# Kernel optimization log

Measured on AMD Instinct MI355X. Metric: run time of the kernel, lower is better.

Reference implementation:

```python
import jax, jax.numpy as jnp
import numpy as np

EPS_LN = 1e-6  # ieps_ln_default


def setup_inputs() -> dict:
    key = jax.random.key(0)
    ks = jax.random.split(key, 8)
    B, S, H, ID = 8, 2048, 8, 256  # batch, seq, heads, i_head_dim
    OD = 256                        # o_head_dim
    sc_hid = 1.0 / np.sqrt(2 * ID)
    sc_og = 1.0 / np.sqrt(ID + OD)
    return {
        "heads_input": jax.random.normal(ks[0], (B, S, H, ID), dtype=jnp.float32),
        "W_hid": jax.random.uniform(ks[1], (3 * OD, 2 * ID), jnp.float32, -sc_hid, sc_hid),
        "b_hid": jnp.zeros((3 * OD,), jnp.float32),
        "W_og": jax.random.uniform(ks[2], (OD, ID + OD), jnp.float32, -sc_og, sc_og),
        "b_og": jnp.zeros((OD,), jnp.float32),
        "ln_w": jnp.ones((H, ID), jnp.float32),
        "ln_b": jnp.zeros((H, ID), jnp.float32),
        "init_cx": jnp.zeros((H, OD), jnp.float32),
    }


def _forward(heads_input, W_hid, b_hid, W_og, b_og, ln_w, ln_b, init_cx):
    B, S, H, ID = heads_input.shape
    OD = init_cx.shape[-1]
    # RS1cumsumstatnorm: causal running sum, LayerNorm over (heads, dim) jointly
    csum = jnp.cumsum(heads_input, axis=1)
    mean = jnp.mean(csum, axis=(-2, -1), keepdims=True)
    var = jnp.var(csum, axis=(-2, -1), keepdims=True)
    csum = (csum - mean) * jax.lax.rsqrt(var + EPS_LN) * ln_w + ln_b
    # trans_hid on cat(input, csum): [B,S,H,2*ID] -> [B,S,H,3*OD]
    x2 = jnp.concatenate([heads_input, csum], axis=-1)
    g = jnp.einsum('bshd,od->bsho', x2, W_hid) + b_hid
    g = g.reshape(B, S, H, 3, OD)
    igate, fgate, hidden = g[..., 0, :], g[..., 1, :], g[..., 2, :]
    fgate = jax.nn.sigmoid(fgate)
    igh = jax.nn.sigmoid(igate) * jax.nn.relu(hidden)
    # LGateFunc: cell_t = f_t * cell_{t-1} + igh_t, starting from init_cx
    c0 = jnp.broadcast_to(init_cx, (B, H, OD))

    def step(c, fi):
        f, ig = fi
        c = f * c + ig
        return c, c

    _, cells = jax.lax.scan(step, c0, (jnp.moveaxis(fgate, 1, 0), jnp.moveaxis(igh, 1, 0)))
    cell = jnp.moveaxis(cells, 0, 1)  # [B,S,H,OD]
    # output gate on cat(input, cell)
    xo = jnp.concatenate([heads_input, cell], axis=-1)
    og = jax.nn.sigmoid(jnp.einsum('bshd,od->bsho', xo, W_og) + b_og)
    return og * cell


def reference(heads_input, W_hid, b_hid, W_og, b_og, ln_w, ln_b, init_cx):
    return _forward(heads_input, W_hid, b_hid, W_og, b_og, ln_w, ln_b, init_cx)
```

## Files before the change

kernel.cpp:

```cpp
#include <hip/hip_runtime.h>

typedef unsigned short u16;
typedef unsigned int u32;

typedef __attribute__((ext_vector_type(8))) short bf16x8;
typedef __attribute__((ext_vector_type(4))) float f32x4;

#define B_ 8
#define S_ 2048
#define H_ 8
#define ID_ 256
#define OD_ 256
#define K_ 512
#define M_ (B_*S_*H_)
#define N1_ 768
#define N2_ 256
#define G2_ 512

#define CSCH 64
#define CSST (S_/CSCH)

#define OFF_X2   (0ull)
#define SZ_X2    ((unsigned long long)M_*K_*2)
#define OFF_G    (OFF_X2 + SZ_X2)
#define SZ_G     ((unsigned long long)M_*G2_*2)
#define OFF_WH   (OFF_G + SZ_G)
#define SZ_WH    ((unsigned long long)N1_*K_*2)
#define OFF_WO   (OFF_WH + SZ_WH)
#define SZ_WO    ((unsigned long long)N2_*K_*2)
#define OFF_AUX  (OFF_WO + SZ_WO)
#define SZ_AUX   ((unsigned long long)B_*CSCH*2048*4)
#define OFF_CF   (OFF_AUX + SZ_AUX)
#define SZ_CARR  ((unsigned long long)B_*H_*32*256*4)
#define OFF_CC   (OFF_CF + SZ_CARR)
#define OFF_CIN  (OFF_CC + SZ_CARR)
#define OFF_BR   (OFF_CIN + SZ_CARR)
#define SZ_BR    ((unsigned long long)N1_*4)

__device__ __forceinline__ u16 f2bf(float f) {
    union { float f; u32 u; } v; v.f = f;
    u32 u = v.u;
    u += 0x7fffu + ((u >> 16) & 1u);
    return (u16)(u >> 16);
}
__device__ __forceinline__ float bf2f(u16 h) {
    union { u32 u; float f; } v; v.u = ((u32)h) << 16;
    return v.f;
}
__device__ __forceinline__ u32 pack2h(float a, float b) {
    union { _Float16 h; u16 u; } x, y;
    x.h = (_Float16)a; y.h = (_Float16)b;
    return (u32)x.u | ((u32)y.u << 16);
}
__device__ __forceinline__ float h2f(u16 u) {
    union { u16 u; _Float16 h; } v; v.u = u;
    return (float)v.h;
}
__device__ __forceinline__ float sigm(float x) {
    return 1.0f / (1.0f + __expf(-x));
}

__device__ __forceinline__ void gld16(const void* g, void* l) {
    __builtin_amdgcn_global_load_lds(
        (const __attribute__((address_space(1))) void*)g,
        (__attribute__((address_space(3))) void*)l, 16, 0, 0);
}

__device__ __forceinline__ int whid_src_row(int n) {
    if (n < 512) {
        int o = ((n >> 7) << 6) + ((n & 127) >> 1);
        return (n & 1) ? (512 + o) : o;
    }
    return 256 + (n - 512);
}

__global__ __launch_bounds__(256) void wconv_kernel(
    const float* __restrict__ Whid, const float* __restrict__ bhid,
    const float* __restrict__ Wog,
    u16* __restrict__ WhB, u16* __restrict__ WoB, float* __restrict__ br)
{
    int idx = blockIdx.x * 256 + threadIdx.x;
    if (idx < N1_*K_) {
        const int n = idx >> 9, k = idx & 511;
        WhB[idx] = f2bf(Whid[(size_t)whid_src_row(n) * K_ + k]);
    }
    if (idx < N2_*K_) WoB[idx] = f2bf(Wog[idx]);
    if (idx < N1_) br[idx] = bhid[whid_src_row(idx)];
}

__global__ __launch_bounds__(256) void csum_phase1(
    const float* __restrict__ X, float* __restrict__ aux)
{
    const int bch = blockIdx.x;
    const int b = bch / CSCH, ch = bch % CSCH;
    const int t = threadIdx.x;
    float acc[8];
#pragma unroll
    for (int h = 0; h < 8; ++h) acc[h] = 0.f;
    for (int i = 0; i < CSST; ++i) {
        const int s = ch * CSST + i;
        const float* xp = X + ((size_t)(b * S_ + s)) * 2048 + t;
#pragma unroll
        for (int h = 0; h < 8; ++h) acc[h] += xp[h * 256];
    }
    float* ap = aux + (size_t)bch * 2048 + t;
#pragma unroll
    for (int h = 0; h < 8; ++h) ap[h * 256] = acc[h];
}

__global__ __launch_bounds__(256) void csum_mid(float* __restrict__ aux)
{
    const int idx = blockIdx.x * 256 + threadIdx.x;
    const int b = idx >> 11, c = idx & 2047;
    float run = 0.f;
    for (int ch = 0; ch < CSCH; ++ch) {
        float* p = aux + ((size_t)(b * CSCH + ch)) * 2048 + c;
        float v = *p; *p = run; run += v;
    }
}

__global__ __launch_bounds__(256) void csum_phase2(
    const float* __restrict__ X, const float* __restrict__ aux,
    const float* __restrict__ lnw, const float* __restrict__ lnb,
    u16* __restrict__ x2)
{
    const int bch = blockIdx.x;
    const int b = bch / CSCH, ch = bch % CSCH;
    const int t = threadIdx.x;
    float c[8], wv[8], bv[8];
#pragma unroll
    for (int h = 0; h < 8; ++h) {
        c[h]  = aux[(size_t)bch * 2048 + h * 256 + t];
        wv[h] = lnw[h * 256 + t];
        bv[h] = lnb[h * 256 + t];
    }
    __shared__ float red[2][4];
    for (int i = 0; i < CSST; ++i) {
        const int s = ch * CSST + i;
        const float* xp = X + ((size_t)(b * S_ + s)) * 2048 + t;
        float xa[8];
#pragma unroll
        for (int h = 0; h < 8; ++h) { xa[h] = xp[h * 256]; c[h] += xa[h]; }
        float sx = 0.f, sq = 0.f;
#pragma unroll
        for (int h = 0; h < 8; ++h) { sx += c[h]; sq += c[h] * c[h]; }
#pragma unroll
        for (int off = 32; off >= 1; off >>= 1) {
            sx += __shfl_down(sx, (unsigned)off);
            sq += __shfl_down(sq, (unsigned)off);
        }
        const int wid = t >> 6;
        if ((t & 63) == 0) { red[0][wid] = sx; red[1][wid] = sq; }
        __syncthreads();
        const float tsx = red[0][0] + red[0][1] + red[0][2] + red[0][3];
        const float tsq = red[1][0] + red[1][1] + red[1][2] + red[1][3];
        __syncthreads();
        const float mean = tsx * (1.f / 2048.f);
        const float var  = tsq * (1.f / 2048.f) - mean * mean;
        const float rstd = rsqrtf(var + 1e-6f);
        const size_t mrow = ((size_t)(b * S_ + s)) * H_;
#pragma unroll
        for (int h = 0; h < 8; ++h) {
            u16* row = x2 + (mrow + h) * (size_t)K_;
            row[t]       = f2bf(xa[h]);
            row[256 + t] = f2bf((c[h] - mean) * rstd * wv[h] + bv[h]);
        }
    }
}

template<int N, int EPI>
__global__ __launch_bounds__(256) void gemm_kernel(
    const u16* __restrict__ A, const u16* __restrict__ Bw,
    u16* __restrict__ Gout, const float* __restrict__ bias,
    const u16* __restrict__ cellbuf, float* __restrict__ Out)
{
    constexpr int NT = N / 128;
    const int blk = blockIdx.x;
    const int xcd = blk & 7;
    const int j = blk >> 3;
    const int tileN = j % NT;
    const int tileM = (j / NT) * 8 + xcd;
    const int m0 = tileM * 128, n0 = tileN * 128;
    const int tid = threadIdx.x;
    const int lane = tid & 63;
    const int w = tid >> 6, wm = w & 1, wn = w >> 1;
    const int l15 = lane & 15, quad = lane >> 4;

    __shared__ __align__(16) u16 smem[2 * 128 * 64];
    u16* As = smem;
    u16* Bs = smem + 128 * 64;

    const int lane3 = lane >> 3;
    const int pc = lane & 7;
    const int ra7 = l15 & 7;

    f32x4 acc[4][4];
    const f32x4 zero4 = {0.f, 0.f, 0.f, 0.f};
#pragma unroll
    for (int i = 0; i < 4; ++i)
#pragma unroll
        for (int jj = 0; jj < 4; ++jj) acc[i][jj] = zero4;

    for (int kt = 0; kt < K_ / 64; ++kt) {
        const int k0 = kt * 64;
#pragma unroll
        for (int p = 0; p < 4; ++p) {
            const int R0 = w * 32 + p * 8;
            const int r = R0 + lane3;
            const int ca = (pc ^ (r & 7)) * 8;
            gld16(A  + (size_t)(m0 + r) * K_ + k0 + ca, As + R0 * 64);
            gld16(Bw + (size_t)(n0 + r) * K_ + k0 + ca, Bs + R0 * 64);
        }
        asm volatile("s_waitcnt vmcnt(0)" ::: "memory");
        __syncthreads();
#pragma unroll
        for (int kk = 0; kk < 2; ++kk) {
            bf16x8 af[4], bfr[4];
#pragma unroll
            for (int i = 0; i < 4; ++i) {
                const int rowa = wm * 64 + i * 16 + l15;
                const int rowb = wn * 64 + i * 16 + l15;
                const int ca = ((kk * 4 + quad) ^ ra7) * 8;
                af[i]  = *(const bf16x8*)(const void*)(&As[rowa * 64 + ca]);
                bfr[i] = *(const bf16x8*)(const void*)(&Bs[rowb * 64 + ca]);
            }
#pragma unroll
            for (int i = 0; i < 4; ++i)
#pragma unroll
                for (int jj = 0; jj < 4; ++jj)
                    acc[i][jj] = __builtin_amdgcn_mfma_f32_16x16x32_bf16(
                        af[i], bfr[jj], acc[i][jj], 0, 0, 0);
        }
        __syncthreads();
    }

    float* Cf = (float*)smem;
    const int col4 = (tid & 31) * 4;
    float4 b4;
    if (EPI == 0) b4 = *(const float4*)(const void*)(bias + n0 + col4);
    else          b4 = *(const float4*)(const void*)(bias + n0 + col4);
#pragma unroll
    for (int half = 0; half < 2; ++half) {
        if (wm == half) {
#pragma unroll
            for (int i = 0; i < 4; ++i) {
                const int lrow0 = i * 16 + quad * 4;
#pragma unroll
                for (int jj = 0; jj < 4; ++jj) {
                    const int col = wn * 64 + jj * 16 + l15;
#pragma unroll
                    for (int r = 0; r < 4; ++r)
                        Cf[(lrow0 + r) * 128 + col] = acc[i][jj][r];
                }
            }
        }
        __syncthreads();
#pragma unroll
        for (int q = 0; q < 8; ++q) {
            const int lrow = q * 8 + (tid >> 5);
            const int grow = m0 + half * 64 + lrow;
            float4 v = *(const float4*)(const void*)(&Cf[lrow * 128 + col4]);
            if (EPI == 0) {
                if (tileN < 4) {
                    const float ig0 = sigm(v.x + b4.x) * fmaxf(v.y + b4.y, 0.f);
                    const float ig1 = sigm(v.z + b4.z) * fmaxf(v.w + b4.w, 0.f);
                    *(u32*)(void*)(Gout + (size_t)grow * G2_ + tileN * 64 + (col4 >> 1))
                        = pack2h(ig0, ig1);
                } else {
                    uint2 pk;
                    pk.x = pack2h(sigm(v.x + b4.x), sigm(v.y + b4.y));
                    pk.y = pack2h(sigm(v.z + b4.z), sigm(v.w + b4.w));
                    *(uint2*)(void*)(Gout + (size_t)grow * G2_ + 256 + (tileN - 4) * 128 + col4)
                        = pk;
                }
            } else {
                const u16* cp = cellbuf + (size_t)grow * K_ + 256 + n0 + col4;
                float4 o;
                o.x = sigm(v.x + b4.x) * bf2f(cp[0]);
                o.y = sigm(v.y + b4.y) * bf2f(cp[1]);
                o.z = sigm(v.z + b4.z) * bf2f(cp[2]);
                o.w = sigm(v.w + b4.w) * bf2f(cp[3]);
                *(float4*)(void*)(Out + (size_t)grow * N2_ + n0 + col4) = o;
            }
        }
        __syncthreads();
    }
}

__global__ __launch_bounds__(256) void scan_phase1(
    const u16* __restrict__ g2, float* __restrict__ cF, float* __restrict__ cC)
{
    const int blk = blockIdx.x;
    const int chp = blk & 7, bh = blk >> 3;
    const int h = bh & 7, b = bh >> 3;
    const int t = threadIdx.x;
    const int ch = chp * 4 + (t >> 6);
    const int o = (t & 63) * 4;
    float F[4] = {1.f, 1.f, 1.f, 1.f};
    float c[4] = {0.f, 0.f, 0.f, 0.f};
    for (int i = 0; i < 64; ++i) {
        const int s = ch * 64 + i;
        const size_t m = ((size_t)(b * S_ + s)) * H_ + h;
        const u16* gp = g2 + m * G2_;
        const uint2 igp = *(const uint2*)(const void*)(gp + o);
        const uint2 fgp = *(const uint2*)(const void*)(gp + 256 + o);
        const float f0 = h2f((u16)fgp.x), f1 = h2f((u16)(fgp.x >> 16));
        const float f2 = h2f((u16)fgp.y), f3 = h2f((u16)(fgp.y >> 16));
        c[0] = f0 * c[0] + h2f((u16)igp.x);        F[0] *= f0;
        c[1] = f1 * c[1] + h2f((u16)(igp.x >> 16)); F[1] *= f1;
        c[2] = f2 * c[2] + h2f((u16)igp.y);        F[2] *= f2;
        c[3] = f3 * c[3] + h2f((u16)(igp.y >> 16)); F[3] *= f3;
    }
    const size_t idx = ((size_t)(bh * 32 + ch)) * 256 + o;
    *(float4*)(void*)(cF + idx) = make_float4(F[0], F[1], F[2], F[3]);
    *(float4*)(void*)(cC + idx) = make_float4(c[0], c[1], c[2], c[3]);
}

__global__ __launch_bounds__(256) void scan_mid(
    const float* __restrict__ cF, const float* __restrict__ cC,
    const float* __restrict__ initcx, float* __restrict__ cin)
{
    const int bh = blockIdx.x;
    const int h = bh & 7;
    const int o = threadIdx.x;
    float c = initcx[h * 256 + o];
    for (int ch = 0; ch < 32; ++ch) {
        const size_t idx = ((size_t)(bh * 32 + ch)) * 256 + o;
        cin[idx] = c;
        c = cF[idx] * c + cC[idx];
    }
}

__global__ __launch_bounds__(256) void scan_phase2(
    const u16* __restrict__ g2, const float* __restrict__ cin,
    u16* __restrict__ x2)
{
    const int blk = blockIdx.x;
    const int chp = blk & 7, bh = blk >> 3;
    const int h = bh & 7, b = bh >> 3;
    const int t = threadIdx.x;
    const int ch = chp * 4 + (t >> 6);
    const int o = (t & 63) * 4;
    const size_t idx = ((size_t)(bh * 32 + ch)) * 256 + o;
    float4 c4 = *(const float4*)(const void*)(cin + idx);
    float c[4] = {c4.x, c4.y, c4.z, c4.w};
    for (int i = 0; i < 64; ++i) {
        const int s = ch * 64 + i;
        const size_t m = ((size_t)(b * S_ + s)) * H_ + h;
        const u16* gp = g2 + m * G2_;
        const uint2 igp = *(const uint2*)(const void*)(gp + o);
        const uint2 fgp = *(const uint2*)(const void*)(gp + 256 + o);
        const float f0 = h2f((u16)fgp.x), f1 = h2f((u16)(fgp.x >> 16));
        const float f2 = h2f((u16)fgp.y), f3 = h2f((u16)(fgp.y >> 16));
        c[0] = f0 * c[0] + h2f((u16)igp.x);
        c[1] = f1 * c[1] + h2f((u16)(igp.x >> 16));
        c[2] = f2 * c[2] + h2f((u16)igp.y);
        c[3] = f3 * c[3] + h2f((u16)(igp.y >> 16));
        uint2 pk;
        pk.x = (u32)f2bf(c[0]) | ((u32)f2bf(c[1]) << 16);
        pk.y = (u32)f2bf(c[2]) | ((u32)f2bf(c[3]) << 16);
        *(uint2*)(void*)(x2 + m * K_ + 256 + o) = pk;
    }
}

extern "C" void kernel_launch(void* const* d_in, const int* in_sizes, int n_in,
                              void* d_out, int out_size, void* d_ws, size_t ws_size,
                              hipStream_t stream)
{
    const float* X      = (const float*)d_in[0];
    const float* Whid   = (const float*)d_in[1];
    const float* bhid   = (const float*)d_in[2];
    const float* Wog    = (const float*)d_in[3];
    const float* bog    = (const float*)d_in[4];
    const float* lnw    = (const float*)d_in[5];
    const float* lnb    = (const float*)d_in[6];
    const float* initcx = (const float*)d_in[7];
    float* out = (float*)d_out;

    char* ws = (char*)d_ws;
    u16* x2   = (u16*)(ws + OFF_X2);
    u16* g    = (u16*)(ws + OFF_G);
    u16* WhB  = (u16*)(ws + OFF_WH);
    u16* WoB  = (u16*)(ws + OFF_WO);
    float* aux = (float*)(ws + OFF_AUX);
    float* cF  = (float*)(ws + OFF_CF);
    float* cC  = (float*)(ws + OFF_CC);
    float* cin = (float*)(ws + OFF_CIN);
    float* br  = (float*)(ws + OFF_BR);

    wconv_kernel<<<(N1_*K_ + 255) / 256, 256, 0, stream>>>(Whid, bhid, Wog, WhB, WoB, br);
    csum_phase1<<<B_ * CSCH, 256, 0, stream>>>(X, aux);
    csum_mid<<<64, 256, 0, stream>>>(aux);
    csum_phase2<<<B_ * CSCH, 256, 0, stream>>>(X, aux, lnw, lnb, x2);
    gemm_kernel<N1_, 0><<<(M_ / 128) * (N1_ / 128), 256, 0, stream>>>(
        x2, WhB, g, br, nullptr, nullptr);
    scan_phase1<<<B_ * H_ * 8, 256, 0, stream>>>(g, cF, cC);
    scan_mid<<<B_ * H_, 256, 0, stream>>>(cF, cC, initcx, cin);
    scan_phase2<<<B_ * H_ * 8, 256, 0, stream>>>(g, cin, x2);
    gemm_kernel<N2_, 1><<<(M_ / 128) * (N2_ / 128), 256, 0, stream>>>(
        x2, WoB, nullptr, bog, x2, out);
}
```

Baseline: 640.0 us.

## Write first GEMM epilogue straight from registers using permuted gate layout

```diff
diff --git a/kernel.cpp b/kernel.cpp
--- a/kernel.cpp
+++ b/kernel.cpp
@@ -34,8 +34,6 @@
 #define SZ_CARR  ((unsigned long long)B_*H_*32*256*4)
 #define OFF_CC   (OFF_CF + SZ_CARR)
 #define OFF_CIN  (OFF_CC + SZ_CARR)
-#define OFF_BR   (OFF_CIN + SZ_CARR)
-#define SZ_BR    ((unsigned long long)N1_*4)
 
 __device__ __forceinline__ u16 f2bf(float f) {
     union { float f; u32 u; } v; v.f = f;
@@ -67,17 +65,18 @@
 }
 
 __device__ __forceinline__ int whid_src_row(int n) {
-    if (n < 512) {
-        int o = ((n >> 7) << 6) + ((n & 127) >> 1);
-        return (n & 1) ? (512 + o) : o;
-    }
-    return 256 + (n - 512);
+    const int t = n >> 7, c = n & 127;
+    if (t < 4) {
+        const int wn = (c >> 6) & 1, jj = (c & 63) >> 4, l = c & 15;
+        const int o = t * 64 + wn * 32 + (jj & 1) * 16 + l;
+        return (jj < 2) ? o : (512 + o);
+    }
+    return 256 + (t - 4) * 128 + c;
 }
 
 __global__ __launch_bounds__(256) void wconv_kernel(
-    const float* __restrict__ Whid, const float* __restrict__ bhid,
-    const float* __restrict__ Wog,
-    u16* __restrict__ WhB, u16* __restrict__ WoB, float* __restrict__ br)
+    const float* __restrict__ Whid, const float* __restrict__ Wog,
+    u16* __restrict__ WhB, u16* __restrict__ WoB)
 {
     int idx = blockIdx.x * 256 + threadIdx.x;
     if (idx < N1_*K_) {
@@ -85,7 +84,6 @@
         WhB[idx] = f2bf(Whid[(size_t)whid_src_row(n) * K_ + k]);
     }
     if (idx < N2_*K_) WoB[idx] = f2bf(Wog[idx]);
-    if (idx < N1_) br[idx] = bhid[whid_src_row(idx)];
 }
 
 __global__ __launch_bounds__(256) void csum_phase1(
@@ -234,46 +232,67 @@
         __syncthreads();
     }
 
-    float* Cf = (float*)smem;
-    const int col4 = (tid & 31) * 4;
-    float4 b4;
-    if (EPI == 0) b4 = *(const float4*)(const void*)(bias + n0 + col4);
-    else          b4 = *(const float4*)(const void*)(bias + n0 + col4);
-#pragma unroll
-    for (int half = 0; half < 2; ++half) {
-        if (wm == half) {
+    if (EPI == 0) {
+        const int m_base = m0 + wm * 64 + quad * 4;
+        if (tileN < 4) {
+            const int o0 = tileN * 64 + wn * 32 + l15;
+            const float bI0 = bias[o0],        bI1 = bias[o0 + 16];
+            const float bH0 = bias[512 + o0],  bH1 = bias[512 + o0 + 16];
+            const int q = (tileN * 2 + wn) * 16 + l15;
 #pragma unroll
             for (int i = 0; i < 4; ++i) {
-                const int lrow0 = i * 16 + quad * 4;
-#pragma unroll
-                for (int jj = 0; jj < 4; ++jj) {
-                    const int col = wn * 64 + jj * 16 + l15;
-#pragma unroll
-                    for (int r = 0; r < 4; ++r)
-                        Cf[(lrow0 + r) * 128 + col] = acc[i][jj][r];
+#pragma unroll
+                for (int r = 0; r < 4; ++r) {
+                    const int m = m_base + i * 16 + r;
+                    const float ig0 = sigm(acc[i][0][r] + bI0) * fmaxf(acc[i][2][r] + bH0, 0.f);
+                    const float ig1 = sigm(acc[i][1][r] + bI1) * fmaxf(acc[i][3][r] + bH1, 0.f);
+                    *(u32*)(void*)(Gout + (size_t)m * G2_ + 2 * q) = pack2h(ig0, ig1);
                 }
             }
-        }
-        __syncthreads();
-#pragma unroll
-        for (int q = 0; q < 8; ++q) {
-            const int lrow = q * 8 + (tid >> 5);
-            const int grow = m0 + half * 64 + lrow;
-            float4 v = *(const float4*)(const void*)(&Cf[lrow * 128 + col4]);
-            if (EPI == 0) {
-                if (tileN < 4) {
-                    const float ig0 = sigm(v.x + b4.x) * fmaxf(v.y + b4.y, 0.f);
-                    const float ig1 = sigm(v.z + b4.z) * fmaxf(v.w + b4.w, 0.f);
-                    *(u32*)(void*)(Gout + (size_t)grow * G2_ + tileN * 64 + (col4 >> 1))
-                        = pack2h(ig0, ig1);
-                } else {
-                    uint2 pk;
-                    pk.x = pack2h(sigm(v.x + b4.x), sigm(v.y + b4.y));
-                    pk.y = pack2h(sigm(v.z + b4.z), sigm(v.w + b4.w));
-                    *(uint2*)(void*)(Gout + (size_t)grow * G2_ + 256 + (tileN - 4) * 128 + col4)
-                        = pk;
+        } else {
+            const int o0 = (tileN - 4) * 128 + wn * 64 + l15;
+            const float bF0 = bias[256 + o0],      bF1 = bias[256 + o0 + 16];
+            const float bF2 = bias[256 + o0 + 32], bF3 = bias[256 + o0 + 48];
+            const int qA = ((tileN - 4) * 4 + wn * 2) * 16 + l15;
+            const int qB = qA + 16;
+#pragma unroll
+            for (int i = 0; i < 4; ++i) {
+#pragma unroll
+                for (int r = 0; r < 4; ++r) {
+                    const int m = m_base + i * 16 + r;
+                    u16* row = Gout + (size_t)m * G2_ + 256;
+                    *(u32*)(void*)(row + 2 * qA) =
+                        pack2h(sigm(acc[i][0][r] + bF0), sigm(acc[i][1][r] + bF1));
+                    *(u32*)(void*)(row + 2 * qB) =
+                        pack2h(sigm(acc[i][2][r] + bF2), sigm(acc[i][3][r] + bF3));
                 }
-            } else {
+            }
+        }
+    } else {
+        float* Cf = (float*)smem;
+        const int col4 = (tid & 31) * 4;
+        float4 b4 = *(const float4*)(const void*)(bias + n0 + col4);
+#pragma unroll
+        for (int half = 0; half < 2; ++half) {
+            if (wm == half) {
+#pragma unroll
+                for (int i = 0; i < 4; ++i) {
+                    const int lrow0 = i * 16 + quad * 4;
+#pragma unroll
+                    for (int jj = 0; jj < 4; ++jj) {
+                        const int col = wn * 64 + jj * 16 + l15;
+#pragma unroll
+                        for (int r = 0; r < 4; ++r)
+                            Cf[(lrow0 + r) * 128 + col] = acc[i][jj][r];
+                    }
+                }
+            }
+            __syncthreads();
+#pragma unroll
+            for (int q = 0; q < 8; ++q) {
+                const int lrow = q * 8 + (tid >> 5);
+                const int grow = m0 + half * 64 + lrow;
+                float4 v = *(const float4*)(const void*)(&Cf[lrow * 128 + col4]);
                 const u16* cp = cellbuf + (size_t)grow * K_ + 256 + n0 + col4;
                 float4 o;
                 o.x = sigm(v.x + b4.x) * bf2f(cp[0]);
@@ -282,8 +301,8 @@
                 o.w = sigm(v.w + b4.w) * bf2f(cp[3]);
                 *(float4*)(void*)(Out + (size_t)grow * N2_ + n0 + col4) = o;
             }
-        }
-        __syncthreads();
+            __syncthreads();
+        }
     }
 }
 
@@ -306,9 +325,9 @@
         const uint2 fgp = *(const uint2*)(const void*)(gp + 256 + o);
         const float f0 = h2f((u16)fgp.x), f1 = h2f((u16)(fgp.x >> 16));
         const float f2 = h2f((u16)fgp.y), f3 = h2f((u16)(fgp.y >> 16));
-        c[0] = f0 * c[0] + h2f((u16)igp.x);        F[0] *= f0;
+        c[0] = f0 * c[0] + h2f((u16)igp.x);         F[0] *= f0;
         c[1] = f1 * c[1] + h2f((u16)(igp.x >> 16)); F[1] *= f1;
-        c[2] = f2 * c[2] + h2f((u16)igp.y);        F[2] *= f2;
+        c[2] = f2 * c[2] + h2f((u16)igp.y);         F[2] *= f2;
         c[3] = f3 * c[3] + h2f((u16)(igp.y >> 16)); F[3] *= f3;
     }
     const size_t idx = ((size_t)(bh * 32 + ch)) * 256 + o;
@@ -322,10 +341,12 @@
 {
     const int bh = blockIdx.x;
     const int h = bh & 7;
-    const int o = threadIdx.x;
-    float c = initcx[h * 256 + o];
+    const int a = threadIdx.x;
+    const int q = a >> 1, hfl = a & 1;
+    const int ro = ((q >> 4) << 5) + (q & 15) + (hfl << 4);
+    float c = initcx[h * 256 + ro];
     for (int ch = 0; ch < 32; ++ch) {
-        const size_t idx = ((size_t)(bh * 32 + ch)) * 256 + o;
+        const size_t idx = ((size_t)(bh * 32 + ch)) * 256 + a;
         cin[idx] = c;
         c = cF[idx] * c + cC[idx];
     }
@@ -340,7 +361,9 @@
     const int h = bh & 7, b = bh >> 3;
     const int t = threadIdx.x;
     const int ch = chp * 4 + (t >> 6);
-    const int o = (t & 63) * 4;
+    const int z = t & 63;
+    const int o = z * 4;
+    const int oA = ((z >> 3) << 5) + ((z & 7) << 1);
     const size_t idx = ((size_t)(bh * 32 + ch)) * 256 + o;
     float4 c4 = *(const float4*)(const void*)(cin + idx);
     float c[4] = {c4.x, c4.y, c4.z, c4.w};
@@ -356,10 +379,11 @@
         c[1] = f1 * c[1] + h2f((u16)(igp.x >> 16));
         c[2] = f2 * c[2] + h2f((u16)igp.y);
         c[3] = f3 * c[3] + h2f((u16)(igp.y >> 16));
-        uint2 pk;
-        pk.x = (u32)f2bf(c[0]) | ((u32)f2bf(c[1]) << 16);
-        pk.y = (u32)f2bf(c[2]) | ((u32)f2bf(c[3]) << 16);
-        *(uint2*)(void*)(x2 + m * K_ + 256 + o) = pk;
+        u16* xr = x2 + m * K_ + 256;
+        const u32 pkA = (u32)f2bf(c[0]) | ((u32)f2bf(c[2]) << 16);
+        const u32 pkB = (u32)f2bf(c[1]) | ((u32)f2bf(c[3]) << 16);
+        *(u32*)(void*)(xr + oA)      = pkA;
+        *(u32*)(void*)(xr + oA + 16) = pkB;
     }
 }
 
@@ -386,14 +410,13 @@
     float* cF  = (float*)(ws + OFF_CF);
     float* cC  = (float*)(ws + OFF_CC);
     float* cin = (float*)(ws + OFF_CIN);
-    float* br  = (float*)(ws + OFF_BR);
-
-    wconv_kernel<<<(N1_*K_ + 255) / 256, 256, 0, stream>>>(Whid, bhid, Wog, WhB, WoB, br);
+
+    wconv_kernel<<<(N1_*K_ + 255) / 256, 256, 0, stream>>>(Whid, Wog, WhB, WoB);
     csum_phase1<<<B_ * CSCH, 256, 0, stream>>>(X, aux);
     csum_mid<<<64, 256, 0, stream>>>(aux);
     csum_phase2<<<B_ * CSCH, 256, 0, stream>>>(X, aux, lnw, lnb, x2);
     gemm_kernel<N1_, 0><<<(M_ / 128) * (N1_ / 128), 256, 0, stream>>>(
-        x2, WhB, g, br, nullptr, nullptr);
+        x2, WhB, g, bhid, nullptr, nullptr);
     scan_phase1<<<B_ * H_ * 8, 256, 0, stream>>>(g, cF, cC);
     scan_mid<<<B_ * H_, 256, 0, stream>>>(cF, cC, initcx, cin);
     scan_phase2<<<B_ * H_ * 8, 256, 0, stream>>>(g, cin, x2);
```

Result: faster. 623.4 us (-2.6%).
